# Kernel optimization log

Hardware: AMD Instinct MI355X
Metric: run time of the kernel (lower is better)

Reference implementation:

```python
import jax, jax.numpy as jnp
import numpy as np

D_MODEL = 1024
N_HEADS = 16
HEAD_DIM = D_MODEL // N_HEADS


def setup_inputs() -> dict:
    key = jax.random.key(0)
    ks = jax.random.split(key, 9)
    B, S = 4, 2048
    x = jax.random.normal(ks[0], (B, S, D_MODEL), dtype=jnp.float32)
    # causal mask, broadcastable to (B, H, S, S); mask==0 -> -inf
    mask = jnp.tril(jnp.ones((S, S), dtype=jnp.int32))[None, None, :, :]
    s = 1.0 / np.sqrt(D_MODEL)
    wq = jax.random.normal(ks[1], (D_MODEL, D_MODEL), dtype=jnp.float32) * s
    wk = jax.random.normal(ks[2], (D_MODEL, D_MODEL), dtype=jnp.float32) * s
    wv = jax.random.normal(ks[3], (D_MODEL, D_MODEL), dtype=jnp.float32) * s
    wo = jax.random.normal(ks[4], (D_MODEL, D_MODEL), dtype=jnp.float32) * s
    bq = jnp.zeros((D_MODEL,), jnp.float32)
    bk = jnp.zeros((D_MODEL,), jnp.float32)
    bv = jnp.zeros((D_MODEL,), jnp.float32)
    bo = jnp.zeros((D_MODEL,), jnp.float32)
    return {"x": x, "mask": mask, "wq": wq, "bq": bq, "wk": wk, "bk": bk,
            "wv": wv, "bv": bv, "wo": wo, "bo": bo}


def reference(x, mask, wq, bq, wk, bk, wv, bv, wo, bo):
    B, S, D = x.shape
    H, Hd = N_HEADS, HEAD_DIM
    # torch nn.Linear: y = x @ W^T + b
    q = (jnp.einsum('bsd,ed->bse', x, wq) + bq).reshape(B, S, H, Hd).transpose(0, 2, 1, 3)
    k = (jnp.einsum('bsd,ed->bse', x, wk) + bk).reshape(B, S, H, Hd).transpose(0, 2, 1, 3)
    v = (jnp.einsum('bsd,ed->bse', x, wv) + bv).reshape(B, S, H, Hd).transpose(0, 2, 1, 3)
    scores = jnp.einsum('bhqd,bhkd->bhqk', q, k) / jnp.sqrt(jnp.float32(Hd))
    scores = jnp.where(mask == 0, -jnp.inf, scores)
    attn = jax.nn.softmax(scores, axis=-1)
    out = jnp.einsum('bhqk,bhkd->bhqd', attn, v)  # (B,H,S,Hd)
    out = out.transpose(0, 2, 1, 3).reshape(B, S, D)
    return jnp.einsum('bsd,ed->bse', out, wo) + bo
```

## Files before the change

### kernel.cpp

```cpp
#include <hip/hip_runtime.h>
#include <hip/hip_bf16.h>
#include <math.h>

using bf16x8 = __attribute__((ext_vector_type(8))) __bf16;
using bf16x4 = __attribute__((ext_vector_type(4))) __bf16;
using f32x4  = __attribute__((ext_vector_type(4))) float;
using f32x16 = __attribute__((ext_vector_type(16))) float;
using u32x4  = __attribute__((ext_vector_type(4))) unsigned;

static constexpr int S_ = 2048;
static constexpr float SCALE_L2E = 0.125f * 1.44269504088896340736f;

__device__ __forceinline__ void gload16(const void* g, void* lds) {
    __builtin_amdgcn_global_load_lds((const __attribute__((address_space(1))) void*)g,
                                     (__attribute__((address_space(3))) void*)lds, 16, 0, 0);
}

__device__ __forceinline__ unsigned pk2(float a, float b) {
    unsigned short lo = __builtin_bit_cast(unsigned short, (__bf16)a);
    unsigned short hi = __builtin_bit_cast(unsigned short, (__bf16)b);
    return (unsigned)lo | ((unsigned)hi << 16);
}

__device__ __forceinline__ float max3f(float a, float b, float c) {
    return fmaxf(fmaxf(a, b), c);
}

__global__ void cast_f32_bf16(const float* __restrict__ src, __bf16* __restrict__ dst, int n4) {
    int i = blockIdx.x * blockDim.x + threadIdx.x;
    if (i < n4) {
        float4 v = reinterpret_cast<const float4*>(src)[i];
        bf16x4 o = { (__bf16)v.x, (__bf16)v.y, (__bf16)v.z, (__bf16)v.w };
        reinterpret_cast<bf16x4*>(dst)[i] = o;
    }
}

template <int EPI>
__global__ __launch_bounds__(256) void gemm_bt(
    const __bf16* __restrict__ A, const __bf16* __restrict__ Bt,
    const float* __restrict__ b0, const float* __restrict__ b1, const float* __restrict__ b2,
    __bf16* __restrict__ Qo, __bf16* __restrict__ Ko, __bf16* __restrict__ Vo,
    float* __restrict__ Fo, int K) {
    __shared__ __align__(16) __bf16 LDS_[3][2][4096];
    const int t = threadIdx.x, l = t & 63, w = t >> 6;
    const int m0 = blockIdx.y * 128, n0 = blockIdx.x * 128;
    const int wm = (w >> 1) * 64, wn = (w & 1) * 64;
    f32x4 acc[4][4] = {};

    const int row0 = t >> 2, cw0 = t & 3;
    const int gc = cw0 ^ ((row0 >> 1) & 3);
    const __bf16* Ag0 = A + (size_t)(m0 + row0) * K + gc * 8;
    const __bf16* Ag1 = A + (size_t)(m0 + row0 + 64) * K + gc * 8;
    const __bf16* Bg0 = Bt + (size_t)(n0 + row0) * K + gc * 8;
    const __bf16* Bg1 = Bt + (size_t)(n0 + row0 + 64) * K + gc * 8;
    const int wo512 = w * 512;

#define STAGE(buf, k0)                                          \
    do {                                                        \
        gload16(Ag0 + (k0), &LDS_[buf][0][wo512]);              \
        gload16(Ag1 + (k0), &LDS_[buf][0][2048 + wo512]);       \
        gload16(Bg0 + (k0), &LDS_[buf][1][wo512]);              \
        gload16(Bg1 + (k0), &LDS_[buf][1][2048 + wo512]);       \
    } while (0)

    const int nk = K >> 5;
    STAGE(0, 0);
    STAGE(1, 32);
    int rb = 0, sb = 2;
    const int sc = (l >> 4) ^ ((l >> 1) & 3);
    for (int ki = 0; ki < nk; ++ki) {
        if (ki + 2 < nk) {
            STAGE(sb, (ki + 2) << 5);
            asm volatile("s_waitcnt vmcnt(8)" ::: "memory");
        } else if (ki + 1 < nk) {
            asm volatile("s_waitcnt vmcnt(4)" ::: "memory");
        } else {
            asm volatile("s_waitcnt vmcnt(0)" ::: "memory");
        }
        __builtin_amdgcn_s_barrier();
        const char* rdA = (const char*)&LDS_[rb][0][0];
        const char* rdB = (const char*)&LDS_[rb][1][0];
        bf16x8 af[4], bf[4];
#pragma unroll
        for (int i = 0; i < 4; ++i)
            af[i] = *reinterpret_cast<const bf16x8*>(rdA + (wm + i * 16 + (l & 15)) * 64 + sc * 16);
#pragma unroll
        for (int j = 0; j < 4; ++j)
            bf[j] = *reinterpret_cast<const bf16x8*>(rdB + (wn + j * 16 + (l & 15)) * 64 + sc * 16);
#pragma unroll
        for (int i = 0; i < 4; ++i)
#pragma unroll
            for (int j = 0; j < 4; ++j)
                acc[i][j] = __builtin_amdgcn_mfma_f32_16x16x32_bf16(af[i], bf[j], acc[i][j], 0, 0, 0);
        __builtin_amdgcn_s_barrier();
        rb = (rb == 2) ? 0 : rb + 1;
        sb = (sb == 2) ? 0 : sb + 1;
    }
#undef STAGE

    if (EPI == 0) {
        const int cls = n0 >> 10;
        if (cls < 2) {
            const float* bias = (cls == 0) ? b0 : b1;
#pragma unroll
            for (int j = 0; j < 4; ++j) {
                const int e = n0 + wn + j * 16 + (l & 15);
                const int eh = e & 1023;
                const int h = eh >> 6, hd = eh & 63;
                const float bv = bias[eh];
#pragma unroll
                for (int i = 0; i < 4; ++i)
#pragma unroll
                    for (int r = 0; r < 4; ++r) {
                        const int m = m0 + wm + i * 16 + ((l >> 4) << 2) + r;
                        const int b = m >> 11, s = m & 2047;
                        float v = acc[i][j][r] + bv;
                        if (cls == 0) v *= SCALE_L2E;
                        __bf16* dst = (cls == 0) ? Qo : Ko;
                        dst[((size_t)(b * 16 + h) * 2048 + s) * 64 + hd] = (__bf16)v;
                    }
            }
        } else {
            char* Tr = (char*)&LDS_[0][0][0];
#pragma unroll
            for (int j = 0; j < 4; ++j) {
                const int el = wn + j * 16 + (l & 15);
                const float bv = b2[(n0 & 1023) + el];
#pragma unroll
                for (int i = 0; i < 4; ++i) {
                    const int m4 = wm + i * 16 + ((l >> 4) << 2);
                    const int pos0 = (m4 & 112) | ((m4 & 4) << 1) | ((m4 & 8) >> 1);
                    bf16x4 pkv = { (__bf16)(acc[i][j][0] + bv), (__bf16)(acc[i][j][1] + bv),
                                   (__bf16)(acc[i][j][2] + bv), (__bf16)(acc[i][j][3] + bv) };
                    const int byt = el * 256 + ((pos0 * 2) ^ ((el & 7) << 4));
                    *reinterpret_cast<bf16x4*>(Tr + byt) = pkv;
                }
            }
            __syncthreads();
            const int b = m0 >> 11, sblk = m0 & 2047;
#pragma unroll
            for (int rr = 0; rr < 8; ++rr) {
                const int er = w * 32 + rr * 4 + (l >> 4);
                const int c = l & 15;
                const int slot = c ^ (er & 7);
                bf16x8 vv = *reinterpret_cast<const bf16x8*>(Tr + er * 256 + slot * 16);
                const int eg = (n0 & 1023) + er;
                const int h = eg >> 6, hd = eg & 63;
                char* dst = (char*)(Vo + ((size_t)(b * 16 + h) * 64 + hd) * 2048 + sblk) + c * 16;
                *reinterpret_cast<bf16x8*>(dst) = vv;
            }
        }
    } else {
#pragma unroll
        for (int j = 0; j < 4; ++j) {
            const int e = n0 + wn + j * 16 + (l & 15);
            const float bv = b0[e];
#pragma unroll
            for (int i = 0; i < 4; ++i)
#pragma unroll
                for (int r = 0; r < 4; ++r) {
                    const int m = m0 + wm + i * 16 + ((l >> 4) << 2) + r;
                    Fo[(size_t)m * 1024 + e] = acc[i][j][r] + bv;
                }
        }
    }
}

__global__ __launch_bounds__(256, 4) void attn_fwd(
    const __bf16* __restrict__ Qb, const __bf16* __restrict__ Kb,
    const __bf16* __restrict__ VTb, __bf16* __restrict__ Ob) {
    __shared__ __align__(16) __bf16 Ks[2][64 * 64];
    __shared__ __align__(16) __bf16 Vs[2][64 * 64];
    const int t = threadIdx.x, l = t & 63, w = t >> 6;
    const int id = blockIdx.x;
    const int r = id >> 8, g = (id >> 6) & 3;
    const int qt = (r & 1) ? (2 * g + (r >> 1)) : (15 - 2 * g - (r >> 1));
    const int bh = id & 63;
    const int b = bh >> 4, hh = bh & 15;
    const int hl = l >> 5, l31 = l & 31;

    const __bf16* Qg = Qb + (size_t)bh * S_ * 64;
    const __bf16* Kg = Kb + (size_t)bh * S_ * 64;
    const __bf16* Vg = VTb + (size_t)bh * 64 * S_;

    const int qs = qt * 128 + w * 32;
    const int qg = qs + l31;

    const int tr = t >> 3, sl = t & 7;
    const int swz = (sl ^ (tr & 7)) * 8;
    const __bf16* Ksrc0 = Kg + (size_t)tr * 64 + swz;
    const __bf16* Ksrc1 = Kg + (size_t)(tr + 32) * 64 + swz;
    const __bf16* Vsrc0 = Vg + (size_t)tr * S_ + swz;
    const __bf16* Vsrc1 = Vg + (size_t)(tr + 32) * S_ + swz;
    __bf16* Kd[2] = { &Ks[0][t * 8], &Ks[1][t * 8] };
    __bf16* Vd[2] = { &Vs[0][t * 8], &Vs[1][t * 8] };

#define STAGEKV(cc, kt)                                       \
    do {                                                      \
        gload16(Ksrc0 + (size_t)(kt) * 4096, Kd[cc]);         \
        gload16(Ksrc1 + (size_t)(kt) * 4096, Kd[cc] + 2048);  \
        gload16(Vsrc0 + (kt) * 64, Vd[cc]);                   \
        gload16(Vsrc1 + (kt) * 64, Vd[cc] + 2048);            \
    } while (0)

    bf16x8 qf[4];
#pragma unroll
    for (int c = 0; c < 4; ++c)
        qf[c] = *reinterpret_cast<const bf16x8*>(Qg + (size_t)qg * 64 + c * 16 + hl * 8);

    f32x16 o0 = {}, o1 = {};
    float m_r = -INFINITY, l_r = 0.f;

    const int nkt = 2 * qt + 2;
    STAGEKV(0, 0);
    int cur = 0;
    for (int kt = 0; kt < nkt; ++kt) {
        if (kt + 1 < nkt) {
            STAGEKV(cur ^ 1, kt + 1);
            asm volatile("s_waitcnt vmcnt(4)" ::: "memory");
        } else {
            asm volatile("s_waitcnt vmcnt(0)" ::: "memory");
        }
        __builtin_amdgcn_s_barrier();
        const char* kb = (const char*)(cur ? Ks[1] : Ks[0]);
        const char* vb = (const char*)(cur ? Vs[1] : Vs[0]);
        const int ktb = kt * 64;
        if (ktb <= qs + 31) {
            const int xs = (l & 7) << 4;
            f32x16 s0 = {}, s1 = {};
            __builtin_amdgcn_s_setprio(1);
#pragma unroll
            for (int c = 0; c < 4; ++c) {
                bf16x8 kf0 = *reinterpret_cast<const bf16x8*>(kb + l31 * 128 + ((c * 32 + hl * 16) ^ xs));
                s0 = __builtin_amdgcn_mfma_f32_32x32x16_bf16(kf0, qf[c], s0, 0, 0, 0);
            }
#pragma unroll
            for (int c = 0; c < 4; ++c) {
                bf16x8 kf1 = *reinterpret_cast<const bf16x8*>(kb + (32 + l31) * 128 + ((c * 32 + hl * 16) ^ xs));
                s1 = __builtin_amdgcn_mfma_f32_32x32x16_bf16(kf1, qf[c], s1, 0, 0, 0);
            }
            __builtin_amdgcn_s_setprio(0);
            float p0[16], p1[16];
            const bool bnd = (ktb + 63) > qs;
            if (bnd) {
#pragma unroll
                for (int rr = 0; rr < 16; ++rr) {
                    const int kvr = ktb + (rr & 3) + 8 * (rr >> 2) + 4 * hl;
                    p0[rr] = (kvr > qg) ? -INFINITY : s0[rr];
                    p1[rr] = (kvr + 32 > qg) ? -INFINITY : s1[rr];
                }
            } else {
#pragma unroll
                for (int rr = 0; rr < 16; ++rr) { p0[rr] = s0[rr]; p1[rr] = s1[rr]; }
            }
            float mx[16];
#pragma unroll
            for (int rr = 0; rr < 16; ++rr) mx[rr] = fmaxf(p0[rr], p1[rr]);
            float u0 = max3f(mx[0], mx[1], mx[2]);
            float u1 = max3f(mx[3], mx[4], mx[5]);
            float u2 = max3f(mx[6], mx[7], mx[8]);
            float u3 = max3f(mx[9], mx[10], mx[11]);
            float u4 = max3f(mx[12], mx[13], mx[14]);
            float mt = fmaxf(max3f(u0, u1, u2), max3f(u3, u4, mx[15]));
            mt = fmaxf(mt, __shfl_xor(mt, 32));
            if (!__all(mt - m_r <= 8.0f)) {
                const float mn = fmaxf(m_r, mt);
                const float al = exp2f(m_r - mn);
                m_r = mn;
                l_r *= al;
#pragma unroll
                for (int rr = 0; rr < 16; ++rr) { o0[rr] *= al; o1[rr] *= al; }
            }
            float sm[16];
#pragma unroll
            for (int rr = 0; rr < 16; ++rr) {
                p0[rr] = exp2f(p0[rr] - m_r);
                p1[rr] = exp2f(p1[rr] - m_r);
                sm[rr] = p0[rr] + p1[rr];
            }
#pragma unroll
            for (int s2 = 8; s2 > 0; s2 >>= 1)
#pragma unroll
                for (int rr = 0; rr < 8; ++rr) if (rr < s2) sm[rr] += sm[rr + s2];
            l_r += sm[0] + __shfl_xor(sm[0], 32);
            u32x4 w0 = { pk2(p0[0], p0[1]), pk2(p0[2], p0[3]), pk2(p0[4], p0[5]), pk2(p0[6], p0[7]) };
            u32x4 w1 = { pk2(p0[8], p0[9]), pk2(p0[10], p0[11]), pk2(p0[12], p0[13]), pk2(p0[14], p0[15]) };
            u32x4 w2 = { pk2(p1[0], p1[1]), pk2(p1[2], p1[3]), pk2(p1[4], p1[5]), pk2(p1[6], p1[7]) };
            u32x4 w3 = { pk2(p1[8], p1[9]), pk2(p1[10], p1[11]), pk2(p1[12], p1[13]), pk2(p1[14], p1[15]) };
            bf16x8 pf0 = __builtin_bit_cast(bf16x8, w0);
            bf16x8 pf1 = __builtin_bit_cast(bf16x8, w1);
            bf16x8 pf2 = __builtin_bit_cast(bf16x8, w2);
            bf16x8 pf3 = __builtin_bit_cast(bf16x8, w3);
            __builtin_amdgcn_s_setprio(1);
#pragma unroll
            for (int a = 0; a < 2; ++a) {
                const int rb2 = (a * 32 + l31) * 128;
                bf16x8 vf0 = *reinterpret_cast<const bf16x8*>(vb + rb2 + ((0 * 32 + hl * 16) ^ xs));
                bf16x8 vf1 = *reinterpret_cast<const bf16x8*>(vb + rb2 + ((1 * 32 + hl * 16) ^ xs));
                bf16x8 vf2 = *reinterpret_cast<const bf16x8*>(vb + rb2 + ((2 * 32 + hl * 16) ^ xs));
                bf16x8 vf3 = *reinterpret_cast<const bf16x8*>(vb + rb2 + ((3 * 32 + hl * 16) ^ xs));
                if (a == 0) {
                    o0 = __builtin_amdgcn_mfma_f32_32x32x16_bf16(vf0, pf0, o0, 0, 0, 0);
                    o0 = __builtin_amdgcn_mfma_f32_32x32x16_bf16(vf1, pf1, o0, 0, 0, 0);
                    o0 = __builtin_amdgcn_mfma_f32_32x32x16_bf16(vf2, pf2, o0, 0, 0, 0);
                    o0 = __builtin_amdgcn_mfma_f32_32x32x16_bf16(vf3, pf3, o0, 0, 0, 0);
                } else {
                    o1 = __builtin_amdgcn_mfma_f32_32x32x16_bf16(vf0, pf0, o1, 0, 0, 0);
                    o1 = __builtin_amdgcn_mfma_f32_32x32x16_bf16(vf1, pf1, o1, 0, 0, 0);
                    o1 = __builtin_amdgcn_mfma_f32_32x32x16_bf16(vf2, pf2, o1, 0, 0, 0);
                    o1 = __builtin_amdgcn_mfma_f32_32x32x16_bf16(vf3, pf3, o1, 0, 0, 0);
                }
            }
            __builtin_amdgcn_s_setprio(0);
        }
        __builtin_amdgcn_s_barrier();
        cur ^= 1;
    }
#undef STAGEKV
    const float inv = 1.0f / l_r;
    __bf16* ob = Ob + (size_t)(b * 2048 + qg) * 1024 + hh * 64;
#pragma unroll
    for (int gq = 0; gq < 4; ++gq) {
        bf16x4 v0 = { (__bf16)(o0[4 * gq + 0] * inv), (__bf16)(o0[4 * gq + 1] * inv),
                      (__bf16)(o0[4 * gq + 2] * inv), (__bf16)(o0[4 * gq + 3] * inv) };
        bf16x4 v1 = { (__bf16)(o1[4 * gq + 0] * inv), (__bf16)(o1[4 * gq + 1] * inv),
                      (__bf16)(o1[4 * gq + 2] * inv), (__bf16)(o1[4 * gq + 3] * inv) };
        *reinterpret_cast<bf16x4*>(ob + 8 * gq + 4 * hl) = v0;
        *reinterpret_cast<bf16x4*>(ob + 32 + 8 * gq + 4 * hl) = v1;
    }
}

extern "C" void kernel_launch(void* const* d_in, const int* in_sizes, int n_in,
                              void* d_out, int out_size, void* d_ws, size_t ws_size,
                              hipStream_t stream) {
    const float* x  = (const float*)d_in[0];
    const float* wq = (const float*)d_in[2];
    const float* bq = (const float*)d_in[3];
    const float* wk = (const float*)d_in[4];
    const float* bk = (const float*)d_in[5];
    const float* wv = (const float*)d_in[6];
    const float* bv = (const float*)d_in[7];
    const float* wo = (const float*)d_in[8];
    const float* bo = (const float*)d_in[9];
    float* out = (float*)d_out;

    char* ws = (char*)d_ws;
    __bf16* xb   = (__bf16*)(ws);
    __bf16* wqkv = (__bf16*)(ws + 16777216);
    __bf16* wob  = (__bf16*)(ws + 23068672);
    __bf16* Qb   = (__bf16*)(ws + 25165824);
    __bf16* Kb   = (__bf16*)(ws + 41943040);
    __bf16* VTb  = (__bf16*)(ws + 58720256);
    __bf16* Ob   = (__bf16*)(ws + 75497472);

    cast_f32_bf16<<<8192, 256, 0, stream>>>(x, xb, 2097152);
    cast_f32_bf16<<<1024, 256, 0, stream>>>(wq, wqkv, 262144);
    cast_f32_bf16<<<1024, 256, 0, stream>>>(wk, wqkv + 1048576, 262144);
    cast_f32_bf16<<<1024, 256, 0, stream>>>(wv, wqkv + 2097152, 262144);
    cast_f32_bf16<<<1024, 256, 0, stream>>>(wo, wob, 262144);

    gemm_bt<0><<<dim3(24, 64), 256, 0, stream>>>(xb, wqkv, bq, bk, bv, Qb, Kb, VTb, nullptr, 1024);
    attn_fwd<<<1024, 256, 0, stream>>>(Qb, Kb, VTb, Ob);
    gemm_bt<1><<<dim3(8, 64), 256, 0, stream>>>(Ob, wob, bo, nullptr, nullptr, nullptr, nullptr, nullptr, out, 1024);
}
```

Measured before the change: 185.2 us.

## Split KV range across two wave groups and pair causal query tiles per block

The attention kernel now launches 512 blocks of 512 threads. Each block handles two query tiles (qt=15-p then qt=p) in sequence, which balances the causal workload across blocks. Within a block, two groups of four waves each process alternating KV tiles (a split-K over the key range). The partial softmax states (m, l, O) are then merged through LDS. The aim is more parallelism per query tile and better load balance, at the cost of extra LDS traffic, barriers for the merge, and higher register and LDS pressure per block.

```diff
diff --git a/kernel.cpp b/kernel.cpp
--- a/kernel.cpp
+++ b/kernel.cpp
@@ -166,168 +166,202 @@
     }
 }
 
-__global__ __launch_bounds__(256, 4) void attn_fwd(
+__global__ __launch_bounds__(512, 4) void attn_fwd(
     const __bf16* __restrict__ Qb, const __bf16* __restrict__ Kb,
     const __bf16* __restrict__ VTb, __bf16* __restrict__ Ob) {
-    __shared__ __align__(16) __bf16 Ks[2][64 * 64];
-    __shared__ __align__(16) __bf16 Vs[2][64 * 64];
+    __shared__ __align__(16) __bf16 Ks[2][2][4096];
+    __shared__ __align__(16) __bf16 Vs[2][2][4096];
     const int t = threadIdx.x, l = t & 63, w = t >> 6;
     const int id = blockIdx.x;
-    const int r = id >> 8, g = (id >> 6) & 3;
-    const int qt = (r & 1) ? (2 * g + (r >> 1)) : (15 - 2 * g - (r >> 1));
     const int bh = id & 63;
+    const int p  = id >> 6;
     const int b = bh >> 4, hh = bh & 15;
     const int hl = l >> 5, l31 = l & 31;
+    const int par = w >> 2, sw = w & 3;
 
     const __bf16* Qg = Qb + (size_t)bh * S_ * 64;
     const __bf16* Kg = Kb + (size_t)bh * S_ * 64;
     const __bf16* Vg = VTb + (size_t)bh * 64 * S_;
 
-    const int qs = qt * 128 + w * 32;
-    const int qg = qs + l31;
-
     const int tr = t >> 3, sl = t & 7;
     const int swz = (sl ^ (tr & 7)) * 8;
-    const __bf16* Ksrc0 = Kg + (size_t)tr * 64 + swz;
-    const __bf16* Ksrc1 = Kg + (size_t)(tr + 32) * 64 + swz;
-    const __bf16* Vsrc0 = Vg + (size_t)tr * S_ + swz;
-    const __bf16* Vsrc1 = Vg + (size_t)(tr + 32) * S_ + swz;
-    __bf16* Kd[2] = { &Ks[0][t * 8], &Ks[1][t * 8] };
-    __bf16* Vd[2] = { &Vs[0][t * 8], &Vs[1][t * 8] };
-
-#define STAGEKV(cc, kt)                                       \
-    do {                                                      \
-        gload16(Ksrc0 + (size_t)(kt) * 4096, Kd[cc]);         \
-        gload16(Ksrc1 + (size_t)(kt) * 4096, Kd[cc] + 2048);  \
-        gload16(Vsrc0 + (kt) * 64, Vd[cc]);                   \
-        gload16(Vsrc1 + (kt) * 64, Vd[cc] + 2048);            \
+    const __bf16* Ksrc = Kg + (size_t)tr * 64 + swz;
+    const __bf16* Vsrc = Vg + (size_t)tr * S_ + swz;
+
+#define STAGEKV(cc, i2)                                                      \
+    do {                                                                     \
+        gload16(Ksrc + (size_t)(2 * (i2)) * 4096, &Ks[cc][0][t * 8]);        \
+        gload16(Ksrc + (size_t)(2 * (i2) + 1) * 4096, &Ks[cc][1][t * 8]);    \
+        gload16(Vsrc + (2 * (i2)) * 64, &Vs[cc][0][t * 8]);                  \
+        gload16(Vsrc + (2 * (i2) + 1) * 64, &Vs[cc][1][t * 8]);              \
     } while (0)
 
-    bf16x8 qf[4];
-#pragma unroll
-    for (int c = 0; c < 4; ++c)
-        qf[c] = *reinterpret_cast<const bf16x8*>(Qg + (size_t)qg * 64 + c * 16 + hl * 8);
-
-    f32x16 o0 = {}, o1 = {};
-    float m_r = -INFINITY, l_r = 0.f;
-
-    const int nkt = 2 * qt + 2;
     STAGEKV(0, 0);
-    int cur = 0;
-    for (int kt = 0; kt < nkt; ++kt) {
-        if (kt + 1 < nkt) {
-            STAGEKV(cur ^ 1, kt + 1);
-            asm volatile("s_waitcnt vmcnt(4)" ::: "memory");
-        } else {
-            asm volatile("s_waitcnt vmcnt(0)" ::: "memory");
-        }
-        __builtin_amdgcn_s_barrier();
-        const char* kb = (const char*)(cur ? Ks[1] : Ks[0]);
-        const char* vb = (const char*)(cur ? Vs[1] : Vs[0]);
-        const int ktb = kt * 64;
-        if (ktb <= qs + 31) {
-            const int xs = (l & 7) << 4;
-            f32x16 s0 = {}, s1 = {};
-            __builtin_amdgcn_s_setprio(1);
-#pragma unroll
-            for (int c = 0; c < 4; ++c) {
-                bf16x8 kf0 = *reinterpret_cast<const bf16x8*>(kb + l31 * 128 + ((c * 32 + hl * 16) ^ xs));
-                s0 = __builtin_amdgcn_mfma_f32_32x32x16_bf16(kf0, qf[c], s0, 0, 0, 0);
-            }
-#pragma unroll
-            for (int c = 0; c < 4; ++c) {
-                bf16x8 kf1 = *reinterpret_cast<const bf16x8*>(kb + (32 + l31) * 128 + ((c * 32 + hl * 16) ^ xs));
-                s1 = __builtin_amdgcn_mfma_f32_32x32x16_bf16(kf1, qf[c], s1, 0, 0, 0);
-            }
-            __builtin_amdgcn_s_setprio(0);
-            float p0[16], p1[16];
-            const bool bnd = (ktb + 63) > qs;
-            if (bnd) {
+
+#pragma unroll 1
+    for (int ph = 0; ph < 2; ++ph) {
+        const int qt = ph ? p : (15 - p);
+        const int qs = qt * 128 + sw * 32;
+        const int qg = qs + l31;
+
+        bf16x8 qf[4];
+#pragma unroll
+        for (int c = 0; c < 4; ++c)
+            qf[c] = *reinterpret_cast<const bf16x8*>(Qg + (size_t)qg * 64 + c * 16 + hl * 8);
+
+        f32x16 o0 = {}, o1 = {};
+        float m_r = -INFINITY, l_r = 0.f;
+
+        const int nit = qt + 1;
+        int cur = 0;
+        for (int i = 0; i < nit; ++i) {
+            if (i + 1 < nit) {
+                STAGEKV(cur ^ 1, i + 1);
+                asm volatile("s_waitcnt vmcnt(4)" ::: "memory");
+            } else {
+                asm volatile("s_waitcnt vmcnt(0)" ::: "memory");
+            }
+            __builtin_amdgcn_s_barrier();
+            const char* kb = (const char*)&Ks[cur][par][0];
+            const char* vb = (const char*)&Vs[cur][par][0];
+            const int kt = 2 * i + par, ktb = kt * 64;
+            if (ktb <= qs + 31) {
+                const int xs = (l & 7) << 4;
+                f32x16 s0 = {}, s1 = {};
+                __builtin_amdgcn_s_setprio(1);
+#pragma unroll
+                for (int c = 0; c < 4; ++c) {
+                    bf16x8 kf0 = *reinterpret_cast<const bf16x8*>(kb + l31 * 128 + ((c * 32 + hl * 16) ^ xs));
+                    s0 = __builtin_amdgcn_mfma_f32_32x32x16_bf16(kf0, qf[c], s0, 0, 0, 0);
+                }
+#pragma unroll
+                for (int c = 0; c < 4; ++c) {
+                    bf16x8 kf1 = *reinterpret_cast<const bf16x8*>(kb + (32 + l31) * 128 + ((c * 32 + hl * 16) ^ xs));
+                    s1 = __builtin_amdgcn_mfma_f32_32x32x16_bf16(kf1, qf[c], s1, 0, 0, 0);
+                }
+                __builtin_amdgcn_s_setprio(0);
+                float p0[16], p1[16];
+                const bool bnd = (ktb + 63) > qs;
+                if (bnd) {
+#pragma unroll
+                    for (int rr = 0; rr < 16; ++rr) {
+                        const int kvr = ktb + (rr & 3) + 8 * (rr >> 2) + 4 * hl;
+                        p0[rr] = (kvr > qg) ? -INFINITY : s0[rr];
+                        p1[rr] = (kvr + 32 > qg) ? -INFINITY : s1[rr];
+                    }
+                } else {
+#pragma unroll
+                    for (int rr = 0; rr < 16; ++rr) { p0[rr] = s0[rr]; p1[rr] = s1[rr]; }
+                }
+                float mx[16];
+#pragma unroll
+                for (int rr = 0; rr < 16; ++rr) mx[rr] = fmaxf(p0[rr], p1[rr]);
+                float u0 = max3f(mx[0], mx[1], mx[2]);
+                float u1 = max3f(mx[3], mx[4], mx[5]);
+                float u2 = max3f(mx[6], mx[7], mx[8]);
+                float u3 = max3f(mx[9], mx[10], mx[11]);
+                float u4 = max3f(mx[12], mx[13], mx[14]);
+                float mt = fmaxf(max3f(u0, u1, u2), max3f(u3, u4, mx[15]));
+                mt = fmaxf(mt, __shfl_xor(mt, 32));
+                if (!__all(mt - m_r <= 8.0f)) {
+                    const float mn = fmaxf(m_r, mt);
+                    const float al = exp2f(m_r - mn);
+                    m_r = mn;
+                    l_r *= al;
+#pragma unroll
+                    for (int rr = 0; rr < 16; ++rr) { o0[rr] *= al; o1[rr] *= al; }
+                }
+                float sm[16];
 #pragma unroll
                 for (int rr = 0; rr < 16; ++rr) {
-                    const int kvr = ktb + (rr & 3) + 8 * (rr >> 2) + 4 * hl;
-                    p0[rr] = (kvr > qg) ? -INFINITY : s0[rr];
-                    p1[rr] = (kvr + 32 > qg) ? -INFINITY : s1[rr];
-                }
-            } else {
-#pragma unroll
-                for (int rr = 0; rr < 16; ++rr) { p0[rr] = s0[rr]; p1[rr] = s1[rr]; }
-            }
-            float mx[16];
-#pragma unroll
-            for (int rr = 0; rr < 16; ++rr) mx[rr] = fmaxf(p0[rr], p1[rr]);
-            float u0 = max3f(mx[0], mx[1], mx[2]);
-            float u1 = max3f(mx[3], mx[4], mx[5]);
-            float u2 = max3f(mx[6], mx[7], mx[8]);
-            float u3 = max3f(mx[9], mx[10], mx[11]);
-            float u4 = max3f(mx[12], mx[13], mx[14]);
-            float mt = fmaxf(max3f(u0, u1, u2), max3f(u3, u4, mx[15]));
-            mt = fmaxf(mt, __shfl_xor(mt, 32));
-            if (!__all(mt - m_r <= 8.0f)) {
-                const float mn = fmaxf(m_r, mt);
-                const float al = exp2f(m_r - mn);
-                m_r = mn;
-                l_r *= al;
-#pragma unroll
-                for (int rr = 0; rr < 16; ++rr) { o0[rr] *= al; o1[rr] *= al; }
-            }
-            float sm[16];
-#pragma unroll
-            for (int rr = 0; rr < 16; ++rr) {
-                p0[rr] = exp2f(p0[rr] - m_r);
-                p1[rr] = exp2f(p1[rr] - m_r);
-                sm[rr] = p0[rr] + p1[rr];
-            }
-#pragma unroll
-            for (int s2 = 8; s2 > 0; s2 >>= 1)
-#pragma unroll
-                for (int rr = 0; rr < 8; ++rr) if (rr < s2) sm[rr] += sm[rr + s2];
-            l_r += sm[0] + __shfl_xor(sm[0], 32);
-            u32x4 w0 = { pk2(p0[0], p0[1]), pk2(p0[2], p0[3]), pk2(p0[4], p0[5]), pk2(p0[6], p0[7]) };
-            u32x4 w1 = { pk2(p0[8], p0[9]), pk2(p0[10], p0[11]), pk2(p0[12], p0[13]), pk2(p0[14], p0[15]) };
-            u32x4 w2 = { pk2(p1[0], p1[1]), pk2(p1[2], p1[3]), pk2(p1[4], p1[5]), pk2(p1[6], p1[7]) };
-            u32x4 w3 = { pk2(p1[8], p1[9]), pk2(p1[10], p1[11]), pk2(p1[12], p1[13]), pk2(p1[14], p1[15]) };
-            bf16x8 pf0 = __builtin_bit_cast(bf16x8, w0);
-            bf16x8 pf1 = __builtin_bit_cast(bf16x8, w1);
-            bf16x8 pf2 = __builtin_bit_cast(bf16x8, w2);
-            bf16x8 pf3 = __builtin_bit_cast(bf16x8, w3);
-            __builtin_amdgcn_s_setprio(1);
-#pragma unroll
-            for (int a = 0; a < 2; ++a) {
-                const int rb2 = (a * 32 + l31) * 128;
-                bf16x8 vf0 = *reinterpret_cast<const bf16x8*>(vb + rb2 + ((0 * 32 + hl * 16) ^ xs));
-                bf16x8 vf1 = *reinterpret_cast<const bf16x8*>(vb + rb2 + ((1 * 32 + hl * 16) ^ xs));
-                bf16x8 vf2 = *reinterpret_cast<const bf16x8*>(vb + rb2 + ((2 * 32 + hl * 16) ^ xs));
-                bf16x8 vf3 = *reinterpret_cast<const bf16x8*>(vb + rb2 + ((3 * 32 + hl * 16) ^ xs));
-                if (a == 0) {
-                    o0 = __builtin_amdgcn_mfma_f32_32x32x16_bf16(vf0, pf0, o0, 0, 0, 0);
-                    o0 = __builtin_amdgcn_mfma_f32_32x32x16_bf16(vf1, pf1, o0, 0, 0, 0);
-                    o0 = __builtin_amdgcn_mfma_f32_32x32x16_bf16(vf2, pf2, o0, 0, 0, 0);
-                    o0 = __builtin_amdgcn_mfma_f32_32x32x16_bf16(vf3, pf3, o0, 0, 0, 0);
-                } else {
-                    o1 = __builtin_amdgcn_mfma_f32_32x32x16_bf16(vf0, pf0, o1, 0, 0, 0);
-                    o1 = __builtin_amdgcn_mfma_f32_32x32x16_bf16(vf1, pf1, o1, 0, 0, 0);
-                    o1 = __builtin_amdgcn_mfma_f32_32x32x16_bf16(vf2, pf2, o1, 0, 0, 0);
-                    o1 = __builtin_amdgcn_mfma_f32_32x32x16_bf16(vf3, pf3, o1, 0, 0, 0);
-                }
-            }
-            __builtin_amdgcn_s_setprio(0);
-        }
-        __builtin_amdgcn_s_barrier();
-        cur ^= 1;
+                    p0[rr] = exp2f(p0[rr] - m_r);
+                    p1[rr] = exp2f(p1[rr] - m_r);
+                    sm[rr] = p0[rr] + p1[rr];
+                }
+#pragma unroll
+                for (int s2 = 8; s2 > 0; s2 >>= 1)
+#pragma unroll
+                    for (int rr = 0; rr < 8; ++rr) if (rr < s2) sm[rr] += sm[rr + s2];
+                l_r += sm[0] + __shfl_xor(sm[0], 32);
+                u32x4 w0 = { pk2(p0[0], p0[1]), pk2(p0[2], p0[3]), pk2(p0[4], p0[5]), pk2(p0[6], p0[7]) };
+                u32x4 w1 = { pk2(p0[8], p0[9]), pk2(p0[10], p0[11]), pk2(p0[12], p0[13]), pk2(p0[14], p0[15]) };
+                u32x4 w2 = { pk2(p1[0], p1[1]), pk2(p1[2], p1[3]), pk2(p1[4], p1[5]), pk2(p1[6], p1[7]) };
+                u32x4 w3 = { pk2(p1[8], p1[9]), pk2(p1[10], p1[11]), pk2(p1[12], p1[13]), pk2(p1[14], p1[15]) };
+                bf16x8 pf0 = __builtin_bit_cast(bf16x8, w0);
+                bf16x8 pf1 = __builtin_bit_cast(bf16x8, w1);
+                bf16x8 pf2 = __builtin_bit_cast(bf16x8, w2);
+                bf16x8 pf3 = __builtin_bit_cast(bf16x8, w3);
+                __builtin_amdgcn_s_setprio(1);
+#pragma unroll
+                for (int a = 0; a < 2; ++a) {
+                    const int rb2 = (a * 32 + l31) * 128;
+                    bf16x8 vf0 = *reinterpret_cast<const bf16x8*>(vb + rb2 + ((0 * 32 + hl * 16) ^ xs));
+                    bf16x8 vf1 = *reinterpret_cast<const bf16x8*>(vb + rb2 + ((1 * 32 + hl * 16) ^ xs));
+                    bf16x8 vf2 = *reinterpret_cast<const bf16x8*>(vb + rb2 + ((2 * 32 + hl * 16) ^ xs));
+                    bf16x8 vf3 = *reinterpret_cast<const bf16x8*>(vb + rb2 + ((3 * 32 + hl * 16) ^ xs));
+                    if (a == 0) {
+                        o0 = __builtin_amdgcn_mfma_f32_32x32x16_bf16(vf0, pf0, o0, 0, 0, 0);
+                        o0 = __builtin_amdgcn_mfma_f32_32x32x16_bf16(vf1, pf1, o0, 0, 0, 0);
+                        o0 = __builtin_amdgcn_mfma_f32_32x32x16_bf16(vf2, pf2, o0, 0, 0, 0);
+                        o0 = __builtin_amdgcn_mfma_f32_32x32x16_bf16(vf3, pf3, o0, 0, 0, 0);
+                    } else {
+                        o1 = __builtin_amdgcn_mfma_f32_32x32x16_bf16(vf0, pf0, o1, 0, 0, 0);
+                        o1 = __builtin_amdgcn_mfma_f32_32x32x16_bf16(vf1, pf1, o1, 0, 0, 0);
+                        o1 = __builtin_amdgcn_mfma_f32_32x32x16_bf16(vf2, pf2, o1, 0, 0, 0);
+                        o1 = __builtin_amdgcn_mfma_f32_32x32x16_bf16(vf3, pf3, o1, 0, 0, 0);
+                    }
+                }
+                __builtin_amdgcn_s_setprio(0);
+            }
+            __builtin_amdgcn_s_barrier();
+            cur ^= 1;
+        }
+        if (ph == 0) STAGEKV(0, 0);
+        float* oS  = (float*)&Ks[1][0][0];
+        float* mlS = (float*)&Vs[1][0][0];
+        if (par == 1) {
+#pragma unroll
+            for (int rr = 0; rr < 16; ++rr) oS[sw * 1024 + rr * 64 + l] = o0[rr];
+            mlS[sw * 128 + 2 * l] = m_r;
+            mlS[sw * 128 + 2 * l + 1] = l_r;
+        }
+        __syncthreads();
+        float a1 = 1.f, a2 = 0.f;
+        if (par == 0) {
+            const float m2 = mlS[sw * 128 + 2 * l];
+            const float l2 = mlS[sw * 128 + 2 * l + 1];
+            const float mn = fmaxf(m_r, m2);
+            a1 = exp2f(m_r - mn);
+            a2 = exp2f(m2 - mn);
+            m_r = mn;
+            l_r = l_r * a1 + l2 * a2;
+#pragma unroll
+            for (int rr = 0; rr < 16; ++rr) o0[rr] = o0[rr] * a1 + oS[sw * 1024 + rr * 64 + l] * a2;
+        }
+        __syncthreads();
+        if (par == 1) {
+#pragma unroll
+            for (int rr = 0; rr < 16; ++rr) oS[sw * 1024 + rr * 64 + l] = o1[rr];
+        }
+        __syncthreads();
+        if (par == 0) {
+#pragma unroll
+            for (int rr = 0; rr < 16; ++rr) o1[rr] = o1[rr] * a1 + oS[sw * 1024 + rr * 64 + l] * a2;
+            const float inv = 1.0f / l_r;
+            __bf16* ob = Ob + (size_t)(b * 2048 + qg) * 1024 + hh * 64;
+#pragma unroll
+            for (int gq = 0; gq < 4; ++gq) {
+                bf16x4 v0 = { (__bf16)(o0[4 * gq + 0] * inv), (__bf16)(o0[4 * gq + 1] * inv),
+                              (__bf16)(o0[4 * gq + 2] * inv), (__bf16)(o0[4 * gq + 3] * inv) };
+                bf16x4 v1 = { (__bf16)(o1[4 * gq + 0] * inv), (__bf16)(o1[4 * gq + 1] * inv),
+                              (__bf16)(o1[4 * gq + 2] * inv), (__bf16)(o1[4 * gq + 3] * inv) };
+                *reinterpret_cast<bf16x4*>(ob + 8 * gq + 4 * hl) = v0;
+                *reinterpret_cast<bf16x4*>(ob + 32 + 8 * gq + 4 * hl) = v1;
+            }
+        }
+        __syncthreads();
     }
 #undef STAGEKV
-    const float inv = 1.0f / l_r;
-    __bf16* ob = Ob + (size_t)(b * 2048 + qg) * 1024 + hh * 64;
-#pragma unroll
-    for (int gq = 0; gq < 4; ++gq) {
-        bf16x4 v0 = { (__bf16)(o0[4 * gq + 0] * inv), (__bf16)(o0[4 * gq + 1] * inv),
-                      (__bf16)(o0[4 * gq + 2] * inv), (__bf16)(o0[4 * gq + 3] * inv) };
-        bf16x4 v1 = { (__bf16)(o1[4 * gq + 0] * inv), (__bf16)(o1[4 * gq + 1] * inv),
-                      (__bf16)(o1[4 * gq + 2] * inv), (__bf16)(o1[4 * gq + 3] * inv) };
-        *reinterpret_cast<bf16x4*>(ob + 8 * gq + 4 * hl) = v0;
-        *reinterpret_cast<bf16x4*>(ob + 32 + 8 * gq + 4 * hl) = v1;
-    }
 }
 
 extern "C" void kernel_launch(void* const* d_in, const int* in_sizes, int n_in,
@@ -360,6 +394,6 @@
     cast_f32_bf16<<<1024, 256, 0, stream>>>(wo, wob, 262144);
 
     gemm_bt<0><<<dim3(24, 64), 256, 0, stream>>>(xb, wqkv, bq, bk, bv, Qb, Kb, VTb, nullptr, 1024);
-    attn_fwd<<<1024, 256, 0, stream>>>(Qb, Kb, VTb, Ob);
+    attn_fwd<<<512, 512, 0, stream>>>(Qb, Kb, VTb, Ob);
     gemm_bt<1><<<dim3(8, 64), 256, 0, stream>>>(Ob, wob, bo, nullptr, nullptr, nullptr, nullptr, nullptr, out, 1024);
 }
```

Result: no change. 187.2 us (+1.0%).

## Triple-buffer K/V tiles in attention and simplify block-to-qtile mapping

Applied to the files above, without the earlier changes.

The attention kernel's K/V shared-memory staging goes from double to triple buffering, prefetching two tiles ahead with adjusted vmcnt waits. The aim is to hide more global-load latency behind the MFMA work. LDS per block grows from 32KB to 48KB and launch bounds drop from 4 to 3 blocks per CU. The query-tile ordering also changes from an interleaved heavy/light pattern to plain descending order, so the longest causal tiles are dispatched first.

```diff
diff --git a/kernel.cpp b/kernel.cpp
--- a/kernel.cpp
+++ b/kernel.cpp
@@ -166,15 +166,14 @@
     }
 }
 
-__global__ __launch_bounds__(256, 4) void attn_fwd(
+__global__ __launch_bounds__(256, 3) void attn_fwd(
     const __bf16* __restrict__ Qb, const __bf16* __restrict__ Kb,
     const __bf16* __restrict__ VTb, __bf16* __restrict__ Ob) {
-    __shared__ __align__(16) __bf16 Ks[2][64 * 64];
-    __shared__ __align__(16) __bf16 Vs[2][64 * 64];
+    __shared__ __align__(16) __bf16 Ks[3][4096];
+    __shared__ __align__(16) __bf16 Vs[3][4096];
     const int t = threadIdx.x, l = t & 63, w = t >> 6;
     const int id = blockIdx.x;
-    const int r = id >> 8, g = (id >> 6) & 3;
-    const int qt = (r & 1) ? (2 * g + (r >> 1)) : (15 - 2 * g - (r >> 1));
+    const int qt = 15 - (id >> 6);
     const int bh = id & 63;
     const int b = bh >> 4, hh = bh & 15;
     const int hl = l >> 5, l31 = l & 31;
@@ -192,15 +191,13 @@
     const __bf16* Ksrc1 = Kg + (size_t)(tr + 32) * 64 + swz;
     const __bf16* Vsrc0 = Vg + (size_t)tr * S_ + swz;
     const __bf16* Vsrc1 = Vg + (size_t)(tr + 32) * S_ + swz;
-    __bf16* Kd[2] = { &Ks[0][t * 8], &Ks[1][t * 8] };
-    __bf16* Vd[2] = { &Vs[0][t * 8], &Vs[1][t * 8] };
-
-#define STAGEKV(cc, kt)                                       \
-    do {                                                      \
-        gload16(Ksrc0 + (size_t)(kt) * 4096, Kd[cc]);         \
-        gload16(Ksrc1 + (size_t)(kt) * 4096, Kd[cc] + 2048);  \
-        gload16(Vsrc0 + (kt) * 64, Vd[cc]);                   \
-        gload16(Vsrc1 + (kt) * 64, Vd[cc] + 2048);            \
+
+#define STAGEKV(buf, kt)                                        \
+    do {                                                        \
+        gload16(Ksrc0 + (size_t)(kt) * 4096, &Ks[buf][t * 8]);  \
+        gload16(Ksrc1 + (size_t)(kt) * 4096, &Ks[buf][t * 8 + 2048]); \
+        gload16(Vsrc0 + (kt) * 64, &Vs[buf][t * 8]);            \
+        gload16(Vsrc1 + (kt) * 64, &Vs[buf][t * 8 + 2048]);     \
     } while (0)
 
     bf16x8 qf[4];
@@ -213,17 +210,21 @@
 
     const int nkt = 2 * qt + 2;
     STAGEKV(0, 0);
-    int cur = 0;
+    STAGEKV(1, 1);
+    int rb = 0;
     for (int kt = 0; kt < nkt; ++kt) {
-        if (kt + 1 < nkt) {
-            STAGEKV(cur ^ 1, kt + 1);
+        if (kt + 2 < nkt) {
+            const int sb = (rb == 0) ? 2 : rb - 1;
+            STAGEKV(sb, kt + 2);
+            asm volatile("s_waitcnt vmcnt(8)" ::: "memory");
+        } else if (kt + 1 < nkt) {
             asm volatile("s_waitcnt vmcnt(4)" ::: "memory");
         } else {
             asm volatile("s_waitcnt vmcnt(0)" ::: "memory");
         }
         __builtin_amdgcn_s_barrier();
-        const char* kb = (const char*)(cur ? Ks[1] : Ks[0]);
-        const char* vb = (const char*)(cur ? Vs[1] : Vs[0]);
+        const char* kb = (const char*)&Ks[rb][0];
+        const char* vb = (const char*)&Vs[rb][0];
         const int ktb = kt * 64;
         if (ktb <= qs + 31) {
             const int xs = (l & 7) << 4;
@@ -314,7 +315,7 @@
             __builtin_amdgcn_s_setprio(0);
         }
         __builtin_amdgcn_s_barrier();
-        cur ^= 1;
+        rb = (rb == 2) ? 0 : rb + 1;
     }
 #undef STAGEKV
     const float inv = 1.0f / l_r;
```

Measured after the change: 184.4 us. About the same (-0.5%).
